# Performance work log

Hardware: AMD Instinct MI355X
Metric: run time of the kernel (lower is better)

## Reference

```python
import jax, jax.numpy as jnp
import numpy as np

D_IN = 1024
D_OUT = 1024
NUM_HEADS = 16
HEAD_DIM = D_OUT // NUM_HEADS
CONTEXT_LEN = 2048


def setup_inputs() -> dict:
    key = jax.random.key(0)
    ks = jax.random.split(key, 7)
    scale = 0.02
    x = jax.random.normal(ks[0], (2, 2048, D_IN), dtype=jnp.float32)
    Wq = jax.random.normal(ks[1], (D_IN, D_OUT), dtype=jnp.float32) * scale
    bq = jnp.zeros((D_OUT,), dtype=jnp.float32)
    Wk = jax.random.normal(ks[2], (D_IN, D_OUT), dtype=jnp.float32) * scale
    bk = jnp.zeros((D_OUT,), dtype=jnp.float32)
    Wv = jax.random.normal(ks[3], (D_IN, D_OUT), dtype=jnp.float32) * scale
    bv = jnp.zeros((D_OUT,), dtype=jnp.float32)
    return {"x": x, "Wq": Wq, "bq": bq, "Wk": Wk, "bk": bk, "Wv": Wv, "bv": bv}


def reference(x, Wq, bq, Wk, bk, Wv, bv):
    B, S, _ = x.shape
    # QKV projections with bias
    q = x @ Wq + bq  # [B,S,D_OUT]
    k = x @ Wk + bk
    v = x @ Wv + bv
    # split heads -> [B,H,S,Dh]
    def heads(t):
        return t.reshape(B, S, NUM_HEADS, HEAD_DIM).transpose(0, 2, 1, 3)
    q, k, v = heads(q), heads(k), heads(v)
    # raw scores, then additive causal mask (-1e9 on strictly upper triangle),
    # then scale by 1/sqrt(head_dim) AFTER adding mask (matches original code)
    scores = jnp.einsum("bhqd,bhkd->bhqk", q, k)
    causal = jnp.tril(jnp.ones((S, S), dtype=bool))
    add_mask = jnp.where(causal, 0.0, -1e9).astype(scores.dtype)
    scores = scores + add_mask
    weights = jax.nn.softmax(scores / jnp.sqrt(jnp.asarray(HEAD_DIM, scores.dtype)), axis=-1)
    ctx = jnp.einsum("bhqk,bhkd->bhqd", weights, v)  # [B,H,S,Dh]
    return ctx.transpose(0, 2, 1, 3).reshape(B, S, D_OUT)
```

## Files before the change

### kernel.cpp

```cpp
#include <hip/hip_runtime.h>
#include <hip/hip_bf16.h>
#include <stdint.h>

#define D_IN 1024
#define NH 16
#define DH 64
#define SEQ 2048
#define BATCH 2

typedef unsigned short u16;
typedef __attribute__((ext_vector_type(8))) short short8;
typedef __attribute__((ext_vector_type(4))) float f32x4;

__device__ __forceinline__ u16 f2bf(float f) {
    union { float f; uint32_t u; } v; v.f = f;
    uint32_t r = v.u + 0x7FFF + ((v.u >> 16) & 1);
    return (u16)(r >> 16);
}

__device__ __forceinline__ void async16(const u16* g, u16* l) {
    __builtin_amdgcn_global_load_lds(
        (const __attribute__((address_space(1))) void*)g,
        (__attribute__((address_space(3))) void*)l, 16, 0, 0);
}

__global__ __launch_bounds__(256) void convert_x_kernel(
    const float* __restrict__ x, u16* __restrict__ xb)
{
    int i = (blockIdx.x * 256 + threadIdx.x) * 4;
    float4 v = *(const float4*)(x + i);
    union { u16 u[4]; uint2 d; } o;
    o.u[0] = f2bf(v.x); o.u[1] = f2bf(v.y); o.u[2] = f2bf(v.z); o.u[3] = f2bf(v.w);
    *(uint2*)(xb + i) = o.d;
}

__global__ __launch_bounds__(256) void convert_w_kernel(
    const float* __restrict__ Wq, const float* __restrict__ Wk,
    const float* __restrict__ Wv, u16* __restrict__ WT)
{
    __shared__ float tile[64][65];
    const float* W = (blockIdx.z == 0) ? Wq : (blockIdx.z == 1 ? Wk : Wv);
    int k0 = blockIdx.x * 64, n0 = blockIdx.y * 64;
    int c = threadIdx.x & 63, rb = threadIdx.x >> 6;
    #pragma unroll
    for (int p = 0; p < 16; ++p) {
        int r = p * 4 + rb;
        tile[r][c] = W[(size_t)(k0 + r) * 1024 + n0 + c];
    }
    __syncthreads();
    #pragma unroll
    for (int p = 0; p < 16; ++p) {
        int r = p * 4 + rb;
        WT[((size_t)blockIdx.z * 1024 + n0 + r) * 1024 + k0 + c] = f2bf(tile[c][r]);
    }
}

__global__ __launch_bounds__(256) void qkv_gemm_kernel(
    const u16* __restrict__ xb, const u16* __restrict__ WT,
    const float* __restrict__ bq, const float* __restrict__ bk,
    const float* __restrict__ bv,
    u16* __restrict__ Qb, u16* __restrict__ Kb, u16* __restrict__ Vh)
{
    __shared__ u16 As[128 * 32];
    __shared__ u16 Bs[128 * 32];
    const int tid  = threadIdx.x;
    const int wave = tid >> 6, lane = tid & 63;
    const int quad = lane >> 4, l15 = lane & 15;
    const int m0 = blockIdx.y * 128;
    const int n0 = blockIdx.x * 128;

    f32x4 acc[4][4];
    #pragma unroll
    for (int i = 0; i < 4; ++i)
        #pragma unroll
        for (int j = 0; j < 4; ++j)
            acc[i][j] = (f32x4){0.f, 0.f, 0.f, 0.f};

    const int wm = wave & 1, wn = wave >> 1;
    const int srow = wave * 32 + (lane >> 2);
    const int scol = (lane & 3) * 8;

    for (int k0 = 0; k0 < 1024; k0 += 32) {
        #pragma unroll
        for (int t = 0; t < 2; ++t) {
            int row = srow + t * 16;
            async16(xb + (size_t)(m0 + row) * 1024 + k0 + scol, As + row * 32 + scol);
            async16(WT + (size_t)(n0 + row) * 1024 + k0 + scol, Bs + row * 32 + scol);
        }
        __syncthreads();
        short8 af[4], bfr[4];
        #pragma unroll
        for (int f = 0; f < 4; ++f) {
            af[f]  = *(const short8*)(As + (wm * 64 + f * 16 + l15) * 32 + quad * 8);
            bfr[f] = *(const short8*)(Bs + (wn * 64 + f * 16 + l15) * 32 + quad * 8);
        }
        #pragma unroll
        for (int i = 0; i < 4; ++i)
            #pragma unroll
            for (int j = 0; j < 4; ++j)
                acc[i][j] = __builtin_amdgcn_mfma_f32_16x16x32_bf16(af[i], bfr[j], acc[i][j], 0, 0, 0);
        __syncthreads();
    }

    const int mat = n0 >> 10;
    const float* bias = (mat == 0) ? bq : (mat == 1 ? bk : bv);
    u16* dst = (mat == 0) ? Qb : (mat == 1 ? Kb : Vh);
    const int ncb = (n0 & 1023) + wn * 64;
    const int hh = ncb >> 6;
    #pragma unroll
    for (int i = 0; i < 4; ++i) {
        int gm = m0 + wm * 64 + i * 16 + quad * 4;
        int bb = gm >> 11, ss = gm & 2047;
        #pragma unroll
        for (int j = 0; j < 4; ++j) {
            int dh = j * 16 + l15;
            float bval = bias[ncb + dh];
            size_t base = (((size_t)bb * NH + hh) * SEQ + ss) * DH + dh;
            #pragma unroll
            for (int r = 0; r < 4; ++r)
                dst[base + (size_t)r * DH] = f2bf(acc[i][j][r] + bval);
        }
    }
}

__global__ __launch_bounds__(256) void transpose_v_kernel(
    const u16* __restrict__ Vh, u16* __restrict__ Vt)
{
    __shared__ uint32_t tile[64][65];
    int s0 = blockIdx.x * 64;
    size_t bh = blockIdx.y;
    int c = threadIdx.x & 63, rb = threadIdx.x >> 6;
    const u16* src = Vh + (bh * SEQ + s0) * DH;
    #pragma unroll
    for (int p = 0; p < 16; ++p) {
        int r = p * 4 + rb;
        tile[r][c] = src[(size_t)r * DH + c];
    }
    __syncthreads();
    u16* dst = Vt + bh * DH * SEQ + s0;
    #pragma unroll
    for (int p = 0; p < 16; ++p) {
        int d = p * 4 + rb;
        dst[(size_t)d * SEQ + c] = (u16)tile[c][d];
    }
}

__global__ __launch_bounds__(512) void flash_mfma_kernel(
    const u16* __restrict__ Qb, const u16* __restrict__ Kb,
    const u16* __restrict__ Vt, float* __restrict__ out)
{
    __shared__ u16 Ks[2][64 * 64];
    __shared__ u16 Vs[2][64 * 64];
    __shared__ u16 Ps[128 * 72];

    const int tid  = threadIdx.x;
    const int wave = tid >> 6, lane = tid & 63;
    const int quad = lane >> 4, l15 = lane & 15;
    const int qt = (gridDim.x - 1) - blockIdx.x;
    const int h = blockIdx.y, b = blockIdx.z;
    const int q0 = qt * 128;
    const size_t bh = (size_t)b * NH + h;
    const u16* Qp = Qb + bh * SEQ * DH;
    const u16* Kp = Kb + bh * SEQ * DH;
    const u16* Vp = Vt + bh * DH * SEQ;

    const int srow = tid >> 3;
    const int sch  = (tid & 7) ^ (srow & 7);

    const int qrow = q0 + wave * 16 + l15;
    short8 qf0 = *(const short8*)(Qp + (size_t)qrow * DH + quad * 8);
    short8 qf1 = *(const short8*)(Qp + (size_t)qrow * DH + 32 + quad * 8);

    f32x4 O[4];
    #pragma unroll
    for (int f = 0; f < 4; ++f) O[f] = (f32x4){0.f, 0.f, 0.f, 0.f};
    float ls[4] = {0.f, 0.f, 0.f, 0.f};

    const int ntiles = 2 * qt + 2;

    async16(Kp + (size_t)srow * DH + sch * 8, &Ks[0][tid * 8]);
    async16(Vp + (size_t)srow * SEQ + sch * 8, &Vs[0][tid * 8]);
    __syncthreads();

    const float C = 0.1803368801f;

    for (int t = 0; t < ntiles; ++t) {
        const int cur = t & 1;
        if (t + 1 < ntiles) {
            int k1 = (t + 1) * 64;
            async16(Kp + (size_t)(k1 + srow) * DH + sch * 8, &Ks[cur ^ 1][tid * 8]);
            async16(Vp + (size_t)srow * SEQ + k1 + sch * 8, &Vs[cur ^ 1][tid * 8]);
        }
        f32x4 sf[4];
        #pragma unroll
        for (int fj = 0; fj < 4; ++fj) {
            const u16* krow = &Ks[cur][(fj * 16 + l15) * 64];
            short8 b0 = *(const short8*)(krow + ((quad) ^ (l15 & 7)) * 8);
            short8 b1 = *(const short8*)(krow + ((4 + quad) ^ (l15 & 7)) * 8);
            f32x4 s = (f32x4){0.f, 0.f, 0.f, 0.f};
            s = __builtin_amdgcn_mfma_f32_16x16x32_bf16(qf0, b0, s, 0, 0, 0);
            s = __builtin_amdgcn_mfma_f32_16x16x32_bf16(qf1, b1, s, 0, 0, 0);
            sf[fj] = s;
        }
        const int k0 = t * 64;
        const bool masked = (k0 + 63 > q0 + wave * 16);
        #pragma unroll
        for (int fj = 0; fj < 4; ++fj) {
            #pragma unroll
            for (int r = 0; r < 4; ++r) {
                float p = __builtin_amdgcn_exp2f(sf[fj][r] * C);
                if (masked) {
                    int key = k0 + fj * 16 + l15;
                    int qg  = q0 + wave * 16 + quad * 4 + r;
                    p = (key <= qg) ? p : 0.f;
                }
                sf[fj][r] = p;
                ls[r] += p;
            }
        }
        #pragma unroll
        for (int fj = 0; fj < 4; ++fj)
            #pragma unroll
            for (int r = 0; r < 4; ++r)
                Ps[(wave * 16 + quad * 4 + r) * 72 + fj * 16 + l15] = f2bf(sf[fj][r]);

        short8 pa0 = *(const short8*)(&Ps[(wave * 16 + l15) * 72 + quad * 8]);
        short8 pa1 = *(const short8*)(&Ps[(wave * 16 + l15) * 72 + 32 + quad * 8]);
        #pragma unroll
        for (int fo = 0; fo < 4; ++fo) {
            const u16* vrow = &Vs[cur][(fo * 16 + l15) * 64];
            short8 vb0 = *(const short8*)(vrow + ((quad) ^ (l15 & 7)) * 8);
            short8 vb1 = *(const short8*)(vrow + ((4 + quad) ^ (l15 & 7)) * 8);
            O[fo] = __builtin_amdgcn_mfma_f32_16x16x32_bf16(pa0, vb0, O[fo], 0, 0, 0);
            O[fo] = __builtin_amdgcn_mfma_f32_16x16x32_bf16(pa1, vb1, O[fo], 0, 0, 0);
        }
        __syncthreads();
    }

    #pragma unroll
    for (int r = 0; r < 4; ++r) {
        float s = ls[r];
        s += __shfl_xor(s, 1);
        s += __shfl_xor(s, 2);
        s += __shfl_xor(s, 4);
        s += __shfl_xor(s, 8);
        ls[r] = s;
    }
    #pragma unroll
    for (int fo = 0; fo < 4; ++fo)
        #pragma unroll
        for (int r = 0; r < 4; ++r) {
            int s = q0 + wave * 16 + quad * 4 + r;
            out[((size_t)b * SEQ + s) * 1024 + h * DH + fo * 16 + l15] = O[fo][r] / ls[r];
        }
}

extern "C" void kernel_launch(void* const* d_in, const int* in_sizes, int n_in,
                              void* d_out, int out_size, void* d_ws, size_t ws_size,
                              hipStream_t stream) {
    const float* x  = (const float*)d_in[0];
    const float* Wq = (const float*)d_in[1];
    const float* bq = (const float*)d_in[2];
    const float* Wk = (const float*)d_in[3];
    const float* bk = (const float*)d_in[4];
    const float* Wv = (const float*)d_in[5];
    const float* bv = (const float*)d_in[6];
    float* out = (float*)d_out;

    const size_t NX = (size_t)BATCH * SEQ * D_IN;
    const size_t NW = (size_t)3 * D_IN * 1024;
    const size_t NP = (size_t)BATCH * NH * SEQ * DH;
    u16* xb = (u16*)d_ws;
    u16* WT = xb + NX;
    u16* Qb = WT + NW;
    u16* Kb = Qb + NP;
    u16* Vh = Kb + NP;
    u16* Vt = Vh + NP;

    convert_x_kernel<<<NX / 1024, 256, 0, stream>>>(x, xb);
    convert_w_kernel<<<dim3(16, 16, 3), 256, 0, stream>>>(Wq, Wk, Wv, WT);
    qkv_gemm_kernel<<<dim3(24, 32), 256, 0, stream>>>(xb, WT, bq, bk, bv, Qb, Kb, Vh);
    transpose_v_kernel<<<dim3(SEQ / 64, BATCH * NH), 256, 0, stream>>>(Vh, Vt);
    flash_mfma_kernel<<<dim3(SEQ / 128, NH, BATCH), 512, 0, stream>>>(Qb, Kb, Vt, out);
}
```

Before: 184.8 us.

## Merge prep kernels, write V transposed from GEMM, shrink flash tiles to 64 queries

Combines the x and weight conversion kernels into one launch and has the QKV GEMM epilogue write V directly in transposed layout, removing the separate transpose kernel. The softmax scale is folded into Q at projection time, so the flash kernel skips a multiply per score. The flash kernel now uses 64-query blocks with 256 threads, which doubles the grid and balances causal work more finely. It also computes S transposed so P can be stored to LDS with vector writes, and keeps only the diagonal tile masked. Scaling Q before bf16 rounding slightly changes numerics, and the V epilogue writes are strided.

```diff
diff --git a/kernel.cpp b/kernel.cpp
--- a/kernel.cpp
+++ b/kernel.cpp
@@ -12,6 +12,8 @@
 typedef __attribute__((ext_vector_type(8))) short short8;
 typedef __attribute__((ext_vector_type(4))) float f32x4;
 
+#define CSCALE 0.1803368801f
+
 __device__ __forceinline__ u16 f2bf(float f) {
     union { float f; uint32_t u; } v; v.f = f;
     uint32_t r = v.u + 0x7FFF + ((v.u >> 16) & 1);
@@ -24,23 +26,24 @@
         (__attribute__((address_space(3))) void*)l, 16, 0, 0);
 }
 
-__global__ __launch_bounds__(256) void convert_x_kernel(
-    const float* __restrict__ x, u16* __restrict__ xb)
-{
-    int i = (blockIdx.x * 256 + threadIdx.x) * 4;
-    float4 v = *(const float4*)(x + i);
-    union { u16 u[4]; uint2 d; } o;
-    o.u[0] = f2bf(v.x); o.u[1] = f2bf(v.y); o.u[2] = f2bf(v.z); o.u[3] = f2bf(v.w);
-    *(uint2*)(xb + i) = o.d;
-}
-
-__global__ __launch_bounds__(256) void convert_w_kernel(
-    const float* __restrict__ Wq, const float* __restrict__ Wk,
-    const float* __restrict__ Wv, u16* __restrict__ WT)
+__global__ __launch_bounds__(256) void prep_kernel(
+    const float* __restrict__ x, const float* __restrict__ Wq,
+    const float* __restrict__ Wk, const float* __restrict__ Wv,
+    u16* __restrict__ xb, u16* __restrict__ WT)
 {
     __shared__ float tile[64][65];
-    const float* W = (blockIdx.z == 0) ? Wq : (blockIdx.z == 1 ? Wk : Wv);
-    int k0 = blockIdx.x * 64, n0 = blockIdx.y * 64;
+    if (blockIdx.x < 4096) {
+        int i = (blockIdx.x * 256 + threadIdx.x) * 4;
+        float4 v = *(const float4*)(x + i);
+        union { u16 u[4]; uint2 d; } o;
+        o.u[0] = f2bf(v.x); o.u[1] = f2bf(v.y); o.u[2] = f2bf(v.z); o.u[3] = f2bf(v.w);
+        *(uint2*)(xb + i) = o.d;
+        return;
+    }
+    int idx = blockIdx.x - 4096;
+    int mat = idx >> 8, rem = idx & 255;
+    int k0 = (rem & 15) * 64, n0 = (rem >> 4) * 64;
+    const float* W = (mat == 0) ? Wq : (mat == 1 ? Wk : Wv);
     int c = threadIdx.x & 63, rb = threadIdx.x >> 6;
     #pragma unroll
     for (int p = 0; p < 16; ++p) {
@@ -51,7 +54,7 @@
     #pragma unroll
     for (int p = 0; p < 16; ++p) {
         int r = p * 4 + rb;
-        WT[((size_t)blockIdx.z * 1024 + n0 + r) * 1024 + k0 + c] = f2bf(tile[c][r]);
+        WT[((size_t)mat * 1024 + n0 + r) * 1024 + k0 + c] = f2bf(tile[c][r]);
     }
 }
 
@@ -59,7 +62,7 @@
     const u16* __restrict__ xb, const u16* __restrict__ WT,
     const float* __restrict__ bq, const float* __restrict__ bk,
     const float* __restrict__ bv,
-    u16* __restrict__ Qb, u16* __restrict__ Kb, u16* __restrict__ Vh)
+    u16* __restrict__ Qb, u16* __restrict__ Kb, u16* __restrict__ Vt)
 {
     __shared__ u16 As[128 * 32];
     __shared__ u16 Bs[128 * 32];
@@ -103,70 +106,75 @@
     }
 
     const int mat = n0 >> 10;
-    const float* bias = (mat == 0) ? bq : (mat == 1 ? bk : bv);
-    u16* dst = (mat == 0) ? Qb : (mat == 1 ? Kb : Vh);
     const int ncb = (n0 & 1023) + wn * 64;
     const int hh = ncb >> 6;
-    #pragma unroll
-    for (int i = 0; i < 4; ++i) {
-        int gm = m0 + wm * 64 + i * 16 + quad * 4;
-        int bb = gm >> 11, ss = gm & 2047;
-        #pragma unroll
-        for (int j = 0; j < 4; ++j) {
-            int dh = j * 16 + l15;
-            float bval = bias[ncb + dh];
-            size_t base = (((size_t)bb * NH + hh) * SEQ + ss) * DH + dh;
-            #pragma unroll
-            for (int r = 0; r < 4; ++r)
-                dst[base + (size_t)r * DH] = f2bf(acc[i][j][r] + bval);
-        }
-    }
-}
-
-__global__ __launch_bounds__(256) void transpose_v_kernel(
-    const u16* __restrict__ Vh, u16* __restrict__ Vt)
-{
-    __shared__ uint32_t tile[64][65];
-    int s0 = blockIdx.x * 64;
-    size_t bh = blockIdx.y;
-    int c = threadIdx.x & 63, rb = threadIdx.x >> 6;
-    const u16* src = Vh + (bh * SEQ + s0) * DH;
-    #pragma unroll
-    for (int p = 0; p < 16; ++p) {
-        int r = p * 4 + rb;
-        tile[r][c] = src[(size_t)r * DH + c];
-    }
-    __syncthreads();
-    u16* dst = Vt + bh * DH * SEQ + s0;
-    #pragma unroll
-    for (int p = 0; p < 16; ++p) {
-        int d = p * 4 + rb;
-        dst[(size_t)d * SEQ + c] = (u16)tile[c][d];
-    }
-}
-
-__global__ __launch_bounds__(512) void flash_mfma_kernel(
+    if (mat < 2) {
+        const float* bias = (mat == 0) ? bq : bk;
+        u16* dst = (mat == 0) ? Qb : Kb;
+        const float sc = (mat == 0) ? CSCALE : 1.0f;
+        #pragma unroll
+        for (int i = 0; i < 4; ++i) {
+            int gm = m0 + wm * 64 + i * 16 + quad * 4;
+            int bb = gm >> 11, ss = gm & 2047;
+            #pragma unroll
+            for (int j = 0; j < 4; ++j) {
+                int dh = j * 16 + l15;
+                float bval = bias[ncb + dh];
+                size_t base = (((size_t)bb * NH + hh) * SEQ + ss) * DH + dh;
+                #pragma unroll
+                for (int r = 0; r < 4; ++r)
+                    dst[base + (size_t)r * DH] = f2bf((acc[i][j][r] + bval) * sc);
+            }
+        }
+    } else {
+        #pragma unroll
+        for (int i = 0; i < 4; ++i) {
+            int gm = m0 + wm * 64 + i * 16 + quad * 4;
+            int bb = gm >> 11, ss = gm & 2047;
+            #pragma unroll
+            for (int j = 0; j < 4; ++j) {
+                int dh = j * 16 + l15;
+                float bval = bv[ncb + dh];
+                union { u16 u[4]; uint2 d; } o;
+                #pragma unroll
+                for (int r = 0; r < 4; ++r)
+                    o.u[r] = f2bf(acc[i][j][r] + bval);
+                *(uint2*)(Vt + ((size_t)(bb * NH + hh) * DH + dh) * SEQ + ss) = o.d;
+            }
+        }
+    }
+}
+
+__device__ __forceinline__ void stage64(const u16* g0, size_t gstride, u16* lds,
+                                        int wave, int lane)
+{
+    #pragma unroll
+    for (int rnd = 0; rnd < 2; ++rnd) {
+        int row = rnd * 32 + wave * 8 + (lane >> 3);
+        int c = (lane & 7) ^ (row & 7);
+        async16(g0 + (size_t)row * gstride + c * 8, lds + row * 64 + (lane & 7) * 8);
+    }
+}
+
+__global__ __launch_bounds__(256) void flash_mfma_kernel(
     const u16* __restrict__ Qb, const u16* __restrict__ Kb,
     const u16* __restrict__ Vt, float* __restrict__ out)
 {
     __shared__ u16 Ks[2][64 * 64];
     __shared__ u16 Vs[2][64 * 64];
-    __shared__ u16 Ps[128 * 72];
+    __shared__ u16 Ps[64 * 76];
 
     const int tid  = threadIdx.x;
     const int wave = tid >> 6, lane = tid & 63;
     const int quad = lane >> 4, l15 = lane & 15;
     const int qt = (gridDim.x - 1) - blockIdx.x;
     const int h = blockIdx.y, b = blockIdx.z;
-    const int q0 = qt * 128;
+    const int q0 = qt * 64;
     const size_t bh = (size_t)b * NH + h;
     const u16* Qp = Qb + bh * SEQ * DH;
     const u16* Kp = Kb + bh * SEQ * DH;
     const u16* Vp = Vt + bh * DH * SEQ;
 
-    const int srow = tid >> 3;
-    const int sch  = (tid & 7) ^ (srow & 7);
-
     const int qrow = q0 + wave * 16 + l15;
     short8 qf0 = *(const short8*)(Qp + (size_t)qrow * DH + quad * 8);
     short8 qf1 = *(const short8*)(Qp + (size_t)qrow * DH + 32 + quad * 8);
@@ -174,84 +182,84 @@
     f32x4 O[4];
     #pragma unroll
     for (int f = 0; f < 4; ++f) O[f] = (f32x4){0.f, 0.f, 0.f, 0.f};
-    float ls[4] = {0.f, 0.f, 0.f, 0.f};
-
-    const int ntiles = 2 * qt + 2;
-
-    async16(Kp + (size_t)srow * DH + sch * 8, &Ks[0][tid * 8]);
-    async16(Vp + (size_t)srow * SEQ + sch * 8, &Vs[0][tid * 8]);
+    float lsum = 0.f;
+
+    const int ntiles = qt + 1;
+    stage64(Kp, DH, Ks[0], wave, lane);
+    stage64(Vp, SEQ, Vs[0], wave, lane);
     __syncthreads();
 
-    const float C = 0.1803368801f;
+    const int xq = l15 & 7;
 
     for (int t = 0; t < ntiles; ++t) {
         const int cur = t & 1;
         if (t + 1 < ntiles) {
             int k1 = (t + 1) * 64;
-            async16(Kp + (size_t)(k1 + srow) * DH + sch * 8, &Ks[cur ^ 1][tid * 8]);
-            async16(Vp + (size_t)srow * SEQ + k1 + sch * 8, &Vs[cur ^ 1][tid * 8]);
+            stage64(Kp + (size_t)k1 * DH, DH, Ks[cur ^ 1], wave, lane);
+            stage64(Vp + k1, SEQ, Vs[cur ^ 1], wave, lane);
         }
         f32x4 sf[4];
         #pragma unroll
         for (int fj = 0; fj < 4; ++fj) {
             const u16* krow = &Ks[cur][(fj * 16 + l15) * 64];
-            short8 b0 = *(const short8*)(krow + ((quad) ^ (l15 & 7)) * 8);
-            short8 b1 = *(const short8*)(krow + ((4 + quad) ^ (l15 & 7)) * 8);
+            short8 k0f = *(const short8*)(krow + (quad ^ xq) * 8);
+            short8 k1f = *(const short8*)(krow + ((4 + quad) ^ xq) * 8);
             f32x4 s = (f32x4){0.f, 0.f, 0.f, 0.f};
-            s = __builtin_amdgcn_mfma_f32_16x16x32_bf16(qf0, b0, s, 0, 0, 0);
-            s = __builtin_amdgcn_mfma_f32_16x16x32_bf16(qf1, b1, s, 0, 0, 0);
+            s = __builtin_amdgcn_mfma_f32_16x16x32_bf16(k0f, qf0, s, 0, 0, 0);
+            s = __builtin_amdgcn_mfma_f32_16x16x32_bf16(k1f, qf1, s, 0, 0, 0);
             sf[fj] = s;
         }
-        const int k0 = t * 64;
-        const bool masked = (k0 + 63 > q0 + wave * 16);
+        if (t == qt) {
+            #pragma unroll
+            for (int fj = 0; fj < 4; ++fj)
+                #pragma unroll
+                for (int r = 0; r < 4; ++r) {
+                    float p = __builtin_amdgcn_exp2f(sf[fj][r]);
+                    int key = fj * 16 + quad * 4 + r;
+                    int qg  = wave * 16 + l15;
+                    p = (key <= qg) ? p : 0.f;
+                    sf[fj][r] = p;
+                    lsum += p;
+                }
+        } else {
+            #pragma unroll
+            for (int fj = 0; fj < 4; ++fj)
+                #pragma unroll
+                for (int r = 0; r < 4; ++r) {
+                    float p = __builtin_amdgcn_exp2f(sf[fj][r]);
+                    sf[fj][r] = p;
+                    lsum += p;
+                }
+        }
         #pragma unroll
         for (int fj = 0; fj < 4; ++fj) {
-            #pragma unroll
-            for (int r = 0; r < 4; ++r) {
-                float p = __builtin_amdgcn_exp2f(sf[fj][r] * C);
-                if (masked) {
-                    int key = k0 + fj * 16 + l15;
-                    int qg  = q0 + wave * 16 + quad * 4 + r;
-                    p = (key <= qg) ? p : 0.f;
-                }
-                sf[fj][r] = p;
-                ls[r] += p;
-            }
-        }
-        #pragma unroll
-        for (int fj = 0; fj < 4; ++fj)
-            #pragma unroll
-            for (int r = 0; r < 4; ++r)
-                Ps[(wave * 16 + quad * 4 + r) * 72 + fj * 16 + l15] = f2bf(sf[fj][r]);
-
-        short8 pa0 = *(const short8*)(&Ps[(wave * 16 + l15) * 72 + quad * 8]);
-        short8 pa1 = *(const short8*)(&Ps[(wave * 16 + l15) * 72 + 32 + quad * 8]);
+            union { u16 u[4]; uint2 d; } o;
+            #pragma unroll
+            for (int r = 0; r < 4; ++r) o.u[r] = f2bf(sf[fj][r]);
+            *(uint2*)(&Ps[(wave * 16 + l15) * 76 + fj * 16 + quad * 4]) = o.d;
+        }
+        short8 pa0 = *(const short8*)(&Ps[(wave * 16 + l15) * 76 + quad * 8]);
+        short8 pa1 = *(const short8*)(&Ps[(wave * 16 + l15) * 76 + 32 + quad * 8]);
         #pragma unroll
         for (int fo = 0; fo < 4; ++fo) {
             const u16* vrow = &Vs[cur][(fo * 16 + l15) * 64];
-            short8 vb0 = *(const short8*)(vrow + ((quad) ^ (l15 & 7)) * 8);
-            short8 vb1 = *(const short8*)(vrow + ((4 + quad) ^ (l15 & 7)) * 8);
+            short8 vb0 = *(const short8*)(vrow + (quad ^ xq) * 8);
+            short8 vb1 = *(const short8*)(vrow + ((4 + quad) ^ xq) * 8);
             O[fo] = __builtin_amdgcn_mfma_f32_16x16x32_bf16(pa0, vb0, O[fo], 0, 0, 0);
             O[fo] = __builtin_amdgcn_mfma_f32_16x16x32_bf16(pa1, vb1, O[fo], 0, 0, 0);
         }
         __syncthreads();
     }
 
-    #pragma unroll
-    for (int r = 0; r < 4; ++r) {
-        float s = ls[r];
-        s += __shfl_xor(s, 1);
-        s += __shfl_xor(s, 2);
-        s += __shfl_xor(s, 4);
-        s += __shfl_xor(s, 8);
-        ls[r] = s;
-    }
+    lsum += __shfl_xor(lsum, 16);
+    lsum += __shfl_xor(lsum, 32);
     #pragma unroll
     for (int fo = 0; fo < 4; ++fo)
         #pragma unroll
         for (int r = 0; r < 4; ++r) {
+            float lq = __shfl(lsum, quad * 4 + r);
             int s = q0 + wave * 16 + quad * 4 + r;
-            out[((size_t)b * SEQ + s) * 1024 + h * DH + fo * 16 + l15] = O[fo][r] / ls[r];
+            out[((size_t)b * SEQ + s) * 1024 + h * DH + fo * 16 + l15] = O[fo][r] / lq;
         }
 }
 
@@ -274,12 +282,9 @@
     u16* WT = xb + NX;
     u16* Qb = WT + NW;
     u16* Kb = Qb + NP;
-    u16* Vh = Kb + NP;
-    u16* Vt = Vh + NP;
-
-    convert_x_kernel<<<NX / 1024, 256, 0, stream>>>(x, xb);
-    convert_w_kernel<<<dim3(16, 16, 3), 256, 0, stream>>>(Wq, Wk, Wv, WT);
-    qkv_gemm_kernel<<<dim3(24, 32), 256, 0, stream>>>(xb, WT, bq, bk, bv, Qb, Kb, Vh);
-    transpose_v_kernel<<<dim3(SEQ / 64, BATCH * NH), 256, 0, stream>>>(Vh, Vt);
-    flash_mfma_kernel<<<dim3(SEQ / 128, NH, BATCH), 512, 0, stream>>>(Qb, Kb, Vt, out);
-}
+    u16* Vt = Kb + NP;
+
+    prep_kernel<<<4096 + 768, 256, 0, stream>>>(x, Wq, Wk, Wv, xb, WT);
+    qkv_gemm_kernel<<<dim3(24, 32), 256, 0, stream>>>(xb, WT, bq, bk, bv, Qb, Kb, Vt);
+    flash_mfma_kernel<<<dim3(SEQ / 64, NH, BATCH), 256, 0, stream>>>(Qb, Kb, Vt, out);
+}
```

New measurement: 201.2 us. +8.9%, slower.
